# Kernel tuning notes

Hardware: AMD Instinct MI355X
Metric: run time of the kernel (lower is better)

The kernel has to match this reference:

```python
import jax, jax.numpy as jnp
import numpy as np
from jax.scipy.special import logsumexp

GAMMA = 1.0  # smoothing parameter
B, T1, T2, D_FEAT = 32, 512, 512, 128


def setup_inputs() -> dict:
    key = jax.random.key(0)
    k1, k2 = jax.random.split(key)
    x = jax.random.normal(k1, (B, T1, D_FEAT), dtype=jnp.float32)
    y = jax.random.normal(k2, (B, T2, D_FEAT), dtype=jnp.float32)
    return {"x": x, "y": y}


def _cosine_dist(x, y):
    # F.normalize(p=2, dim=-1) with eps=1e-12 clamp on the norm
    xn = x / jnp.maximum(jnp.linalg.norm(x, axis=-1, keepdims=True), 1e-12)
    yn = y / jnp.maximum(jnp.linalg.norm(y, axis=-1, keepdims=True), 1e-12)
    return 1.0 - jnp.einsum("btd,bsd->bts", xn, yn)  # [B, T1, T2]


def _soft_dtw(D):
    # Anti-diagonal wavefront DP with soft-min (logsumexp) recurrence.
    b, t1, t2 = D.shape
    R0 = jnp.full((b, t1 + 1, t2 + 1), jnp.inf, dtype=D.dtype).at[:, 0, 0].set(0.0)
    i = jnp.arange(1, t1 + 1)  # fixed-length row indices for every diagonal

    def step(R, k):
        j = k - i                      # column index on anti-diagonal k
        valid = (j >= 1) & (j <= t2)
        jc = jnp.clip(j, 0, t2)        # safe R column index (== j when valid)
        jd = jnp.clip(j - 1, 0, t2)    # safe R column index for j-1
        jm = jnp.clip(j - 1, 0, t2 - 1)
        cost = D[:, i - 1, jm]                 # [B, T1]
        r_diag = R[:, i - 1, jd]
        r_left = R[:, i, jd]
        r_up = R[:, i - 1, jc]
        stacked = jnp.stack([r_diag, r_left, r_up])  # [3, B, T1]
        # mask invalid lanes to 0 so logsumexp never sees all -inf (NaN-safe)
        safe = jnp.where(valid[None, None, :], stacked, 0.0)
        soft_min = -GAMMA * logsumexp(-safe / GAMMA, axis=0)
        old = R[:, i, jc]
        val = jnp.where(valid[None, :], cost + soft_min, old)
        R = R.at[:, i, jc].set(val)
        return R, None

    R, _ = jax.lax.scan(step, R0, jnp.arange(2, t1 + t2 + 1))
    return R[:, t1, t2]  # [B]


def reference(x, y):
    D = _cosine_dist(x, y)
    return _soft_dtw(D)
```

## Files before the change

kernel.cpp:

```cpp
#include <hip/hip_runtime.h>
#include <hip/hip_bf16.h>
#include <cstdint>


#define BT      32
#define TLEN    512
#define DF      128
#define NDIAG   1023
#define BIGV    1e30f
#define INV_LN2 1.44269504088896340f
#define LN2     0.69314718055994531f

typedef short bf16x8 __attribute__((ext_vector_type(8)));
typedef float f32x4  __attribute__((ext_vector_type(4)));

__device__ __forceinline__ unsigned f2bf(float f) {
    unsigned u = __builtin_bit_cast(unsigned, f);
    return (u + 0x7FFFu + ((u >> 16) & 1u)) >> 16;
}

__global__ __launch_bounds__(256) void sdtw_normcast(const float* __restrict__ x,
                                                     const float* __restrict__ y,
                                                     unsigned* __restrict__ ox,
                                                     unsigned* __restrict__ oy) {
    const float* in  = blockIdx.y ? y : x;
    unsigned*    out = blockIdx.y ? oy : ox;
    int row = blockIdx.x * 4 + (threadIdx.x >> 6);
    int t   = threadIdx.x & 63;
    float2 v = reinterpret_cast<const float2*>(in + (size_t)row * DF)[t];
    float s = v.x * v.x + v.y * v.y;
    #pragma unroll
    for (int o = 32; o; o >>= 1) s += __shfl_xor(s, o);
    float scale = 1.0f / fmaxf(sqrtf(s), 1e-12f);
    out[(size_t)row * 64 + t] = f2bf(v.x * scale) | (f2bf(v.y * scale) << 16);
}

#define LDSTRIDE 272

__global__ __launch_bounds__(256) void sdtw_gemm_skew(const unsigned* __restrict__ xnb,
                                                      const unsigned* __restrict__ ynb,
                                                      float* __restrict__ skew) {
    __shared__ short smem[34816];
    char* As = (char*)smem;
    char* Bs = (char*)smem + 34816;

    const int b  = blockIdx.z;
    const int r0 = blockIdx.y * 128;
    const int c0 = blockIdx.x * 128;
    const int tid = threadIdx.x;
    const int wid = tid >> 6, l = tid & 63;
    const int lr = l & 15, lg = l >> 4;

    const char* xg = (const char*)(xnb + ((size_t)b * TLEN + r0) * 64);
    const char* yg = (const char*)(ynb + ((size_t)b * TLEN + c0) * 64);

    #pragma unroll
    for (int p = 0; p < 8; ++p) {
        int idx = p * 256 + tid;
        int row = idx >> 4, u = idx & 15;
        *(uint4*)(As + row * LDSTRIDE + u * 16) = *(const uint4*)(xg + row * 256 + u * 16);
        *(uint4*)(Bs + row * LDSTRIDE + u * 16) = *(const uint4*)(yg + row * 256 + u * 16);
    }
    __syncthreads();

    f32x4 acc[8][2];
    #pragma unroll
    for (int rt = 0; rt < 8; ++rt)
        #pragma unroll
        for (int ct = 0; ct < 2; ++ct) acc[rt][ct] = (f32x4){0.f, 0.f, 0.f, 0.f};

    #pragma unroll
    for (int kb = 0; kb < 4; ++kb) {
        bf16x8 af[8], bf[2];
        #pragma unroll
        for (int rt = 0; rt < 8; ++rt)
            af[rt] = *(const bf16x8*)(As + (rt * 16 + lr) * LDSTRIDE + kb * 64 + lg * 16);
        #pragma unroll
        for (int ct = 0; ct < 2; ++ct)
            bf[ct] = *(const bf16x8*)(Bs + (wid * 32 + ct * 16 + lr) * LDSTRIDE + kb * 64 + lg * 16);
        #pragma unroll
        for (int rt = 0; rt < 8; ++rt)
            #pragma unroll
            for (int ct = 0; ct < 2; ++ct)
                acc[rt][ct] = __builtin_amdgcn_mfma_f32_16x16x32_bf16(af[rt], bf[ct], acc[rt][ct], 0, 0, 0);
    }

    __syncthreads();
    float* cs = (float*)smem;
    #pragma unroll
    for (int rt = 0; rt < 8; ++rt)
        #pragma unroll
        for (int ct = 0; ct < 2; ++ct)
            #pragma unroll
            for (int r = 0; r < 4; ++r) {
                int row = rt * 16 + lg * 4 + r;
                int col = wid * 32 + ct * 16 + lr;
                cs[row * 130 + col] = (1.0f - acc[rt][ct][r]) * INV_LN2;
            }
    __syncthreads();

    float* sk = skew + (size_t)b * (NDIAG * TLEN);
    for (int dd = wid; dd < 255; dd += 4) {
        int lo = max(0, dd - 127), hi = min(127, dd);
        for (int rb = lo; rb <= hi; rb += 64) {
            int rl = rb + l;
            if (rl <= hi)
                sk[(size_t)(r0 + c0 + dd) * TLEN + r0 + rl] = cs[rl * 129 + dd];
        }
    }
}

__device__ __forceinline__ int clampi(int v) {
    return v < 0 ? 0 : (v > NDIAG - 1 ? NDIAG - 1 : v);
}

__device__ __forceinline__ float dpp_shr1_old(float old, float x) {
    return __builtin_bit_cast(float,
        __builtin_amdgcn_update_dpp(__builtin_bit_cast(int, old),
                                    __builtin_bit_cast(int, x),
                                    0x138 , 0xF, 0xF, false));
}

#define PH(s, CC, PN, PO, NQC, MASKED, CLAMPED)                                \
  {                                                                            \
    float up_ = dpp_shr1_old(bd_up, PN);                   \
    float dg_ = dgs;                            \
    float m_   = fminf(fminf(dg_, PN), up_);                                   \
    float mid_ = __builtin_amdgcn_fmed3f(dg_, PN, up_);                        \
    float mx_  = fmaxf(fmaxf(dg_, PN), up_);                                   \
    float e_   = 1.0f + __builtin_amdgcn_exp2f(m_ - mid_)                      \
                      + __builtin_amdgcn_exp2f(m_ - mx_);                      \
    float v_   = CC + m_ - __builtin_amdgcn_logf(e_);                          \
    PO = (MASKED) ? (((unsigned)(vb0 + (s)) < 512u) ? v_ : vBig) : v_;         \
    if (((s) & 3) == 0) bq.x = PO;                                             \
    if (((s) & 3) == 1) bq.y = PO;                                             \
    if (((s) & 3) == 2) bq.z = PO;                                             \
    if (((s) & 3) == 3) { bq.w = PO;                                           \
      if (lt == 63) bnd4[c + 1][(q0 + ((s) >> 2)) & 7] = bq; }                 \
    bd_up = (NQC);                                                             \
    dgs = up_;                                                                 \
    { int kl_ = kd0 + (s) + 8; if (CLAMPED) kl_ = clampi(kl_);                 \
      CC = skb[(size_t)kl_ * TLEN]; }                                          \
  }

#define SEG_BODY(MASKED, CLAMPED)                                              \
    PH(0,  c0, P, Q, nq0.x, MASKED, CLAMPED) PH(1,  c1, Q, P, nq0.y, MASKED, CLAMPED) \
    PH(2,  c2, P, Q, nq0.z, MASKED, CLAMPED) PH(3,  c3, Q, P, nq0.w, MASKED, CLAMPED) \
    PH(4,  c4, P, Q, nq1.x, MASKED, CLAMPED) PH(5,  c5, Q, P, nq1.y, MASKED, CLAMPED) \
    PH(6,  c6, P, Q, nq1.z, MASKED, CLAMPED) PH(7,  c7, Q, P, nq1.w, MASKED, CLAMPED) \
    PH(8,  c0, P, Q, nq2.x, MASKED, CLAMPED) PH(9,  c1, Q, P, nq2.y, MASKED, CLAMPED) \
    PH(10, c2, P, Q, nq2.z, MASKED, CLAMPED) PH(11, c3, Q, P, nq2.w, MASKED, CLAMPED) \
    PH(12, c4, P, Q, nq3.x, MASKED, CLAMPED) PH(13, c5, Q, P, nq3.y, MASKED, CLAMPED) \
    PH(14, c6, P, Q, nq3.z, MASKED, CLAMPED) PH(15, c7, Q, P, nq3.w, MASKED, CLAMPED)

#define PRIME(K)                                                               \
    c0 = skb[(size_t)clampi((K) + 0) * TLEN];                                  \
    c1 = skb[(size_t)clampi((K) + 1) * TLEN];                                  \
    c2 = skb[(size_t)clampi((K) + 2) * TLEN];                                  \
    c3 = skb[(size_t)clampi((K) + 3) * TLEN];                                  \
    c4 = skb[(size_t)clampi((K) + 4) * TLEN];                                  \
    c5 = skb[(size_t)clampi((K) + 5) * TLEN];                                  \
    c6 = skb[(size_t)clampi((K) + 6) * TLEN];                                  \
    c7 = skb[(size_t)clampi((K) + 7) * TLEN];

__global__ __launch_bounds__(512) void sdtw_dp(const float* __restrict__ skew,
                                               float* __restrict__ out) {
    const int b   = blockIdx.x;
    const int tid = threadIdx.x;
    const int ww  = tid >> 6;
    const int c   = ((ww & 3) << 1) | (ww >> 2);
    const int lt  = tid & 63;
    const int row = 64 * c + lt;
    const float* skb = skew + (size_t)b * (NDIAG * TLEN) + row;

    __shared__ float4 bnd4[9][8];
    if (tid < 288) ((float*)bnd4)[tid] = BIGV;

    float P = BIGV, Q = BIGV;
    float vBig  = BIGV;
    float bd_up = BIGV;
    float dgs   = (tid == 0) ? 0.0f : BIGV;
    float4 bq = make_float4(BIGV, BIGV, BIGV, BIGV);

    __syncthreads();

    float c0, c1, c2, c3, c4, c5, c6, c7;
    PRIME(-16 * c)

    for (int s = 0; s < 71; ++s) {
        const int sw  = s - 5 * c;
        const int kd0 = 16 * (s - c);
        const int q0  = (kd0 >> 2) & 7;
        const int vb0 = kd0 - row;

        if (sw >= -1 && sw <= 35) {
            float4 nq0 = bnd4[c][q0];
            float4 nq1 = bnd4[c][(q0 + 1) & 7];
            float4 nq2 = bnd4[c][(q0 + 2) & 7];
            float4 nq3 = bnd4[c][(q0 + 3) & 7];
            if (sw == -1) { PRIME(kd0) }
            if (sw >= 4 && sw <= 31) { SEG_BODY(0, 0) }
            else                     { SEG_BODY(1, 1) }
        } else {
            if (lt == 63) {
                float4 bigq = make_float4(BIGV, BIGV, BIGV, BIGV);
                bnd4[c + 1][q0]           = bigq;
                bnd4[c + 1][(q0 + 1) & 7] = bigq;
                bnd4[c + 1][(q0 + 2) & 7] = bigq;
                bnd4[c + 1][(q0 + 3) & 7] = bigq;
            }
        }
        __syncthreads();
    }

    if (tid == 511) out[b] = Q * LN2;
}

extern "C" void kernel_launch(void* const* d_in, const int* in_sizes, int n_in,
                              void* d_out, int out_size, void* d_ws, size_t ws_size,
                              hipStream_t stream) {
    const float* x = (const float*)d_in[0];
    const float* y = (const float*)d_in[1];
    float* outp = (float*)d_out;

    float*    skew = (float*)d_ws;
    unsigned* xnb  = (unsigned*)(skew + (size_t)16760832);
    unsigned* ynb  = xnb + 1048576;

    sdtw_normcast<<<dim3(BT * TLEN / 4, 2), dim3(256), 0, stream>>>(x, y, xnb, ynb);
    sdtw_gemm_skew<<<dim3(4, 4, BT), dim3(256), 0, stream>>>(xnb, ynb, skew);
    sdtw_dp<<<dim3(BT), dim3(512), 0, stream>>>(skew, outp);
}
```

Measured before the change: 122.6 us.

## Fuse normalization, GEMM skew, and DP into one per-batch kernel

Merges the three kernels into a single launch with one 512-thread block per batch. Each block first normalizes and casts its x/y rows to bf16, then computes all 16 128x128 tiles of the cosine cost with MFMA and writes the skewed layout, then runs the wavefront DP. This removes two kernel launches and inter-kernel gaps but confines the normalization and GEMM phases to only 32 workgroups, losing most of the device parallelism for those stages.

After: 316.7 us. +158.2%, slower.

```diff
diff --git a/kernel.cpp b/kernel.cpp
--- a/kernel.cpp
+++ b/kernel.cpp
@@ -19,97 +19,6 @@
     return (u + 0x7FFFu + ((u >> 16) & 1u)) >> 16;
 }
 
-__global__ __launch_bounds__(256) void sdtw_normcast(const float* __restrict__ x,
-                                                     const float* __restrict__ y,
-                                                     unsigned* __restrict__ ox,
-                                                     unsigned* __restrict__ oy) {
-    const float* in  = blockIdx.y ? y : x;
-    unsigned*    out = blockIdx.y ? oy : ox;
-    int row = blockIdx.x * 4 + (threadIdx.x >> 6);
-    int t   = threadIdx.x & 63;
-    float2 v = reinterpret_cast<const float2*>(in + (size_t)row * DF)[t];
-    float s = v.x * v.x + v.y * v.y;
-    #pragma unroll
-    for (int o = 32; o; o >>= 1) s += __shfl_xor(s, o);
-    float scale = 1.0f / fmaxf(sqrtf(s), 1e-12f);
-    out[(size_t)row * 64 + t] = f2bf(v.x * scale) | (f2bf(v.y * scale) << 16);
-}
-
-#define LDSTRIDE 272
-
-__global__ __launch_bounds__(256) void sdtw_gemm_skew(const unsigned* __restrict__ xnb,
-                                                      const unsigned* __restrict__ ynb,
-                                                      float* __restrict__ skew) {
-    __shared__ short smem[34816];
-    char* As = (char*)smem;
-    char* Bs = (char*)smem + 34816;
-
-    const int b  = blockIdx.z;
-    const int r0 = blockIdx.y * 128;
-    const int c0 = blockIdx.x * 128;
-    const int tid = threadIdx.x;
-    const int wid = tid >> 6, l = tid & 63;
-    const int lr = l & 15, lg = l >> 4;
-
-    const char* xg = (const char*)(xnb + ((size_t)b * TLEN + r0) * 64);
-    const char* yg = (const char*)(ynb + ((size_t)b * TLEN + c0) * 64);
-
-    #pragma unroll
-    for (int p = 0; p < 8; ++p) {
-        int idx = p * 256 + tid;
-        int row = idx >> 4, u = idx & 15;
-        *(uint4*)(As + row * LDSTRIDE + u * 16) = *(const uint4*)(xg + row * 256 + u * 16);
-        *(uint4*)(Bs + row * LDSTRIDE + u * 16) = *(const uint4*)(yg + row * 256 + u * 16);
-    }
-    __syncthreads();
-
-    f32x4 acc[8][2];
-    #pragma unroll
-    for (int rt = 0; rt < 8; ++rt)
-        #pragma unroll
-        for (int ct = 0; ct < 2; ++ct) acc[rt][ct] = (f32x4){0.f, 0.f, 0.f, 0.f};
-
-    #pragma unroll
-    for (int kb = 0; kb < 4; ++kb) {
-        bf16x8 af[8], bf[2];
-        #pragma unroll
-        for (int rt = 0; rt < 8; ++rt)
-            af[rt] = *(const bf16x8*)(As + (rt * 16 + lr) * LDSTRIDE + kb * 64 + lg * 16);
-        #pragma unroll
-        for (int ct = 0; ct < 2; ++ct)
-            bf[ct] = *(const bf16x8*)(Bs + (wid * 32 + ct * 16 + lr) * LDSTRIDE + kb * 64 + lg * 16);
-        #pragma unroll
-        for (int rt = 0; rt < 8; ++rt)
-            #pragma unroll
-            for (int ct = 0; ct < 2; ++ct)
-                acc[rt][ct] = __builtin_amdgcn_mfma_f32_16x16x32_bf16(af[rt], bf[ct], acc[rt][ct], 0, 0, 0);
-    }
-
-    __syncthreads();
-    float* cs = (float*)smem;
-    #pragma unroll
-    for (int rt = 0; rt < 8; ++rt)
-        #pragma unroll
-        for (int ct = 0; ct < 2; ++ct)
-            #pragma unroll
-            for (int r = 0; r < 4; ++r) {
-                int row = rt * 16 + lg * 4 + r;
-                int col = wid * 32 + ct * 16 + lr;
-                cs[row * 130 + col] = (1.0f - acc[rt][ct][r]) * INV_LN2;
-            }
-    __syncthreads();
-
-    float* sk = skew + (size_t)b * (NDIAG * TLEN);
-    for (int dd = wid; dd < 255; dd += 4) {
-        int lo = max(0, dd - 127), hi = min(127, dd);
-        for (int rb = lo; rb <= hi; rb += 64) {
-            int rl = rb + l;
-            if (rl <= hi)
-                sk[(size_t)(r0 + c0 + dd) * TLEN + r0 + rl] = cs[rl * 129 + dd];
-        }
-    }
-}
-
 __device__ __forceinline__ int clampi(int v) {
     return v < 0 ? 0 : (v > NDIAG - 1 ? NDIAG - 1 : v);
 }
@@ -121,10 +30,12 @@
                                     0x138 , 0xF, 0xF, false));
 }
 
+#define LDSTRIDE 272
+
 #define PH(s, CC, PN, PO, NQC, MASKED, CLAMPED)                                \
   {                                                                            \
-    float up_ = dpp_shr1_old(bd_up, PN);                   \
-    float dg_ = dgs;                            \
+    float up_ = dpp_shr1_old(bd_up, PN);                                       \
+    float dg_ = dgs;                                                           \
     float m_   = fminf(fminf(dg_, PN), up_);                                   \
     float mid_ = __builtin_amdgcn_fmed3f(dg_, PN, up_);                        \
     float mx_  = fmaxf(fmaxf(dg_, PN), up_);                                   \
@@ -163,17 +74,110 @@
     c6 = skb[(size_t)clampi((K) + 6) * TLEN];                                  \
     c7 = skb[(size_t)clampi((K) + 7) * TLEN];
 
-__global__ __launch_bounds__(512) void sdtw_dp(const float* __restrict__ skew,
-                                               float* __restrict__ out) {
+__global__ __launch_bounds__(512) void sdtw_fused(const float* __restrict__ x,
+                                                  const float* __restrict__ y,
+                                                  unsigned* __restrict__ xnb,
+                                                  unsigned* __restrict__ ynb,
+                                                  float* __restrict__ skew,
+                                                  float* __restrict__ out) {
+    __shared__ __align__(16) char smem[69632];
+    __shared__ float4 bnd4[9][8];
+
     const int b   = blockIdx.x;
     const int tid = threadIdx.x;
     const int ww  = tid >> 6;
+    const int l   = tid & 63;
+
+    {
+        const float* xb = x + (size_t)b * TLEN * DF;
+        const float* yb = y + (size_t)b * TLEN * DF;
+        unsigned* xo = xnb + (size_t)b * TLEN * 64;
+        unsigned* yo = ynb + (size_t)b * TLEN * 64;
+        for (int i = 0; i < 128; ++i) {
+            int g = ww * 128 + i;
+            const float* src = (g < 512) ? xb + (size_t)g * DF
+                                         : yb + (size_t)(g - 512) * DF;
+            unsigned* dst = (g < 512) ? xo + (size_t)g * 64
+                                      : yo + (size_t)(g - 512) * 64;
+            float2 v = reinterpret_cast<const float2*>(src)[l];
+            float s = v.x * v.x + v.y * v.y;
+            #pragma unroll
+            for (int o = 32; o; o >>= 1) s += __shfl_xor(s, o);
+            float scale = 1.0f / fmaxf(sqrtf(s), 1e-12f);
+            dst[l] = f2bf(v.x * scale) | (f2bf(v.y * scale) << 16);
+        }
+    }
+    __threadfence();
+    __syncthreads();
+
+    {
+        char* As = smem;
+        char* Bs = smem + 34816;
+        const int lr = l & 15, lg = l >> 4;
+        float* sk = skew + (size_t)b * (NDIAG * TLEN);
+
+        for (int tr = 0; tr < 4; ++tr) {
+            for (int tc = 0; tc < 4; ++tc) {
+                const int r0 = tr * 128, c0 = tc * 128;
+                const char* xg = (const char*)(xnb + ((size_t)b * TLEN + r0) * 64);
+                const char* yg = (const char*)(ynb + ((size_t)b * TLEN + c0) * 64);
+
+                #pragma unroll
+                for (int p = 0; p < 4; ++p) {
+                    int idx = p * 512 + tid;
+                    int row = idx >> 4, u = idx & 15;
+                    *(uint4*)(As + row * LDSTRIDE + u * 16) = *(const uint4*)(xg + row * 256 + u * 16);
+                    *(uint4*)(Bs + row * LDSTRIDE + u * 16) = *(const uint4*)(yg + row * 256 + u * 16);
+                }
+                __syncthreads();
+
+                f32x4 acc[8];
+                #pragma unroll
+                for (int rt = 0; rt < 8; ++rt) acc[rt] = (f32x4){0.f, 0.f, 0.f, 0.f};
+
+                #pragma unroll
+                for (int kb = 0; kb < 4; ++kb) {
+                    bf16x8 af[8], bfr;
+                    #pragma unroll
+                    for (int rt = 0; rt < 8; ++rt)
+                        af[rt] = *(const bf16x8*)(As + (rt * 16 + lr) * LDSTRIDE + kb * 64 + lg * 16);
+                    bfr = *(const bf16x8*)(Bs + (ww * 16 + lr) * LDSTRIDE + kb * 64 + lg * 16);
+                    #pragma unroll
+                    for (int rt = 0; rt < 8; ++rt)
+                        acc[rt] = __builtin_amdgcn_mfma_f32_16x16x32_bf16(af[rt], bfr, acc[rt], 0, 0, 0);
+                }
+
+                __syncthreads();
+                float* cs = (float*)smem;
+                #pragma unroll
+                for (int rt = 0; rt < 8; ++rt)
+                    #pragma unroll
+                    for (int r = 0; r < 4; ++r) {
+                        int row = rt * 16 + lg * 4 + r;
+                        int col = ww * 16 + lr;
+                        cs[row * 130 + col] = (1.0f - acc[rt][r]) * INV_LN2;
+                    }
+                __syncthreads();
+
+                for (int dd = ww; dd < 255; dd += 8) {
+                    int lo = max(0, dd - 127), hi = min(127, dd);
+                    for (int rb = lo; rb <= hi; rb += 64) {
+                        int rl = rb + l;
+                        if (rl <= hi)
+                            sk[(size_t)(r0 + c0 + dd) * TLEN + r0 + rl] = cs[rl * 129 + dd];
+                    }
+                }
+                __syncthreads();
+            }
+        }
+    }
+    __threadfence();
+
     const int c   = ((ww & 3) << 1) | (ww >> 2);
-    const int lt  = tid & 63;
+    const int lt  = l;
     const int row = 64 * c + lt;
     const float* skb = skew + (size_t)b * (NDIAG * TLEN) + row;
 
-    __shared__ float4 bnd4[9][8];
     if (tid < 288) ((float*)bnd4)[tid] = BIGV;
 
     float P = BIGV, Q = BIGV;
@@ -227,7 +231,5 @@
     unsigned* xnb  = (unsigned*)(skew + (size_t)16760832);
     unsigned* ynb  = xnb + 1048576;
 
-    sdtw_normcast<<<dim3(BT * TLEN / 4, 2), dim3(256), 0, stream>>>(x, y, xnb, ynb);
-    sdtw_gemm_skew<<<dim3(4, 4, BT), dim3(256), 0, stream>>>(xnb, ynb, skew);
-    sdtw_dp<<<dim3(BT), dim3(512), 0, stream>>>(skew, outp);
-}
+    sdtw_fused<<<dim3(BT), dim3(512), 0, stream>>>(x, y, xnb, ynb, skew, outp);
+}
```
